# Kernel optimization log

Measured on AMD Instinct MI355X. Metric: run time of the kernel, lower is better.

Reference implementation:

```python
import jax, jax.numpy as jnp
import numpy as np

D_MODEL = 1024
N_HEADS = 32
HEAD_DIM = D_MODEL // N_HEADS
EPS = 1e-5


def setup_inputs() -> dict:
    key = jax.random.key(0)
    ks = jax.random.split(key, 6)
    B, S = 2, 2048
    scale = 1.0 / np.sqrt(D_MODEL)
    return {
        "x": jax.random.normal(ks[0], (B, S, D_MODEL), dtype=jnp.float32),
        "Wqkv_w": jax.random.normal(ks[1], (3 * D_MODEL, D_MODEL), dtype=jnp.float32) * scale,
        "Wqkv_b": jax.random.normal(ks[2], (3 * D_MODEL,), dtype=jnp.float32) * 0.01,
        "gn_w": jnp.ones((D_MODEL,), dtype=jnp.float32),
        "gn_b": jnp.zeros((D_MODEL,), dtype=jnp.float32),
        "out_w": jax.random.normal(ks[3], (D_MODEL, D_MODEL), dtype=jnp.float32) * scale,
        "out_b": jax.random.normal(ks[4], (D_MODEL,), dtype=jnp.float32) * 0.01,
    }


def reference(x, Wqkv_w, Wqkv_b, gn_w, gn_b, out_w, out_b):
    B, S, Dm = x.shape
    H, Dh = N_HEADS, HEAD_DIM
    # QKV projection
    qkv = x @ Wqkv_w.T + Wqkv_b                      # [B,S,3*Dm]
    qkv = qkv.reshape(B, S, 3, H, Dh)
    q, k, v = qkv[:, :, 0], qkv[:, :, 1], qkv[:, :, 2]  # each [B,S,H,Dh]
    # Linear (softmax-free) attention; dropout p=0 -> identity
    a = jnp.einsum('bthd,bshd->bhts', q, k)          # [B,H,S,S]
    ctx = jnp.einsum('bhts,bshd->bthd', a, v)        # [B,S,H,Dh]
    # GroupNorm(num_groups=H, num_channels=Dm) on transposed (B, Dm, S):
    # normalizes jointly over (Dh channels, S positions) per (batch, group)
    g = ctx.transpose(0, 2, 3, 1)                    # [B,H,Dh,S]
    mean = g.mean(axis=(2, 3), keepdims=True)
    var = ((g - mean) ** 2).mean(axis=(2, 3), keepdims=True)
    gh = (g - mean) * jax.lax.rsqrt(var + EPS)
    gh = gh * gn_w.reshape(H, Dh, 1) + gn_b.reshape(H, Dh, 1)
    ctx = gh.transpose(0, 3, 1, 2).reshape(B, S, Dm)  # back to [B,S,Dm]
    return ctx @ out_w.T + out_b
```

## Files before the change

### kernel.cpp

```cpp
#include <hip/hip_runtime.h>
#include <hip/hip_bf16.h>
#include <stdint.h>

typedef unsigned short ushort_t;
typedef __attribute__((ext_vector_type(4))) float f32x4;
typedef __attribute__((ext_vector_type(8))) short short8;

#define SS 2048
#define ROWS 4096
#define EPS 1e-5f

__device__ __forceinline__ unsigned short f2bf(float f) {
  unsigned int u = __float_as_uint(f);
  u += 0x7FFF + ((u >> 16) & 1);
  return (unsigned short)(u >> 16);
}
__device__ __forceinline__ float bf2f(short s) {
  return __uint_as_float(((unsigned int)(unsigned short)s) << 16);
}

#define GLDS16(g, l)                                                        \
  __builtin_amdgcn_global_load_lds((__attribute__((address_space(1))) void*)(g), \
                                   (__attribute__((address_space(3))) void*)(l), 16, 0, 0)

__global__ __launch_bounds__(256) void f2b3_kernel(const float* __restrict__ a,
                                                   ushort_t* __restrict__ oa, int n4a,
                                                   const float* __restrict__ b,
                                                   ushort_t* __restrict__ ob, int n4b,
                                                   const float* __restrict__ c,
                                                   ushort_t* __restrict__ oc, int n4c) {
  const int stride = gridDim.x * blockDim.x;
  const int total = n4a + n4b + n4c;
  for (int i = blockIdx.x * blockDim.x + threadIdx.x; i < total; i += stride) {
    const float* src; ushort_t* dst; int idx;
    if (i < n4a)            { src = a; dst = oa; idx = i; }
    else if (i < n4a + n4b) { src = b; dst = ob; idx = i - n4a; }
    else                    { src = c; dst = oc; idx = i - n4a - n4b; }
    const float4 v = reinterpret_cast<const float4*>(src)[idx];
    ushort4 o;
    o.x = f2bf(v.x); o.y = f2bf(v.y); o.z = f2bf(v.z); o.w = f2bf(v.w);
    reinterpret_cast<ushort4*>(dst)[idx] = o;
  }
}

#define MF(d, va, vb) d = __builtin_amdgcn_mfma_f32_16x16x32_bf16(va, vb, d, 0, 0, 0)
#define LD8(p) (*reinterpret_cast<const short8*>(p))

__global__ __launch_bounds__(512, 2) void gemm1_pipe(const ushort_t* __restrict__ A,
                                                     const ushort_t* __restrict__ B,
                                                     const float* __restrict__ bias,
                                                     ushort_t* __restrict__ C) {
  __shared__ __align__(16) ushort_t lds[4 * 14336];
  const int tid = threadIdx.x;
  const int wid = tid >> 6, lane = tid & 63;
  const int lin = blockIdx.x + (blockIdx.y << 4);
  const int xcd = lin & 7, idx = lin >> 3;
  const int bm = (((xcd & 3) << 2) + (idx & 3)) * 256;
  const int bn = (((xcd >> 2) << 3) + (idx >> 2)) * 192;
  const int wm = wid >> 2, wn = wid & 3;

  const int srow = lane >> 2;
  const int scol = ((lane & 3) ^ ((lane >> 3) & 3)) * 8;
  const int widb = (wid < 6) ? wid : 0;
  const ushort_t* gA0 = A + (size_t)(bm + wid * 16 + srow) * 1024 + scol;
  const ushort_t* gA1 = A + (size_t)(bm + (8 + wid) * 16 + srow) * 1024 + scol;
  const ushort_t* gB0 = B + (size_t)(bn + widb * 16 + srow) * 1024 + scol;
  const ushort_t* gB1 = B + (size_t)(bn + (6 + widb) * 16 + srow) * 1024 + scol;

  const int lf = lane & 15, kf = lane >> 4;
  const int flip = ((lane >> 1) & 3) << 4;
  const int aBase = (((wm * 128 + lf) * 64 + kf * 16) ^ flip) >> 1;
  const int bBase = ((((wn * 48 + lf) * 64 + kf * 16) ^ flip) >> 1) + 8192;

  f32x4 acc[8][3] = {};

#define STAGE_A(t)                                                           \
  { ushort_t* d = lds + (((t) & 3) * 14336);                                 \
    GLDS16(gA0 + (t) * 32, d + wid * 512);                                   \
    GLDS16(gA1 + (t) * 32, d + (8 + wid) * 512); }
#define STAGE_B(t)                                                           \
  if (wid < 6) { ushort_t* d = lds + (((t) & 3) * 14336) + 8192;             \
    GLDS16(gB0 + (t) * 32, d + wid * 512);                                   \
    GLDS16(gB1 + (t) * 32, d + (6 + wid) * 512); }

  STAGE_A(0) STAGE_B(0)
  STAGE_A(1) STAGE_B(1)
  STAGE_A(2) STAGE_B(2)
  if (wid < 6) { asm volatile("s_waitcnt vmcnt(8)" ::: "memory"); }
  else         { asm volatile("s_waitcnt vmcnt(4)" ::: "memory"); }
  __builtin_amdgcn_s_barrier();
  __builtin_amdgcn_sched_barrier(0);

#define K_TILE(t, DO_STAGE, VM6, VM2)                                        \
  { const ushort_t* Lb = lds + (((t) & 3) * 14336);                          \
    short8 bv0 = LD8(Lb + bBase);                                            \
    short8 bv1 = LD8(Lb + bBase + 512);                                      \
    short8 bv2 = LD8(Lb + bBase + 1024);                                     \
    short8 a0 = LD8(Lb + aBase);                                             \
    short8 a1 = LD8(Lb + aBase + 512);                                       \
    short8 a2 = LD8(Lb + aBase + 1024);                                      \
    short8 a3 = LD8(Lb + aBase + 1536);                                      \
    if (DO_STAGE) STAGE_A((t) + 3)                                           \
    __builtin_amdgcn_s_setprio(1);                                           \
    MF(acc[0][0], a0, bv0); MF(acc[1][0], a1, bv0);                          \
    MF(acc[0][1], a0, bv1); MF(acc[1][1], a1, bv1);                          \
    MF(acc[0][2], a0, bv2); MF(acc[1][2], a1, bv2);                          \
    MF(acc[2][0], a2, bv0); MF(acc[3][0], a3, bv0);                          \
    MF(acc[2][1], a2, bv1); MF(acc[3][1], a3, bv1);                          \
    MF(acc[2][2], a2, bv2); MF(acc[3][2], a3, bv2);                          \
    __builtin_amdgcn_s_setprio(0);                                           \
    a0 = LD8(Lb + aBase + 2048);                                             \
    a1 = LD8(Lb + aBase + 2560);                                             \
    a2 = LD8(Lb + aBase + 3072);                                             \
    a3 = LD8(Lb + aBase + 3584);                                             \
    if (DO_STAGE) STAGE_B((t) + 3)                                           \
    __builtin_amdgcn_s_setprio(1);                                           \
    MF(acc[4][0], a0, bv0); MF(acc[5][0], a1, bv0);                          \
    MF(acc[4][1], a0, bv1); MF(acc[5][1], a1, bv1);                          \
    MF(acc[4][2], a0, bv2); MF(acc[5][2], a1, bv2);                          \
    MF(acc[6][0], a2, bv0); MF(acc[7][0], a3, bv0);                          \
    MF(acc[6][1], a2, bv1); MF(acc[7][1], a3, bv1);                          \
    MF(acc[6][2], a2, bv2); MF(acc[7][2], a3, bv2);                          \
    __builtin_amdgcn_s_setprio(0);                                           \
    __builtin_amdgcn_sched_barrier(0);                                       \
    if (wid < 6) { asm volatile("s_waitcnt vmcnt(" #VM6 ")" ::: "memory"); } \
    else         { asm volatile("s_waitcnt vmcnt(" #VM2 ")" ::: "memory"); } \
    __builtin_amdgcn_s_barrier();                                            \
    __builtin_amdgcn_sched_barrier(0); }

#pragma unroll 1
  for (int t = 0; t < 29; ++t) K_TILE(t, 1, 8, 4)
  K_TILE(29, 0, 4, 2)
  K_TILE(30, 0, 0, 0)
  K_TILE(31, 0, 0, 0)

  const int crow = bm + wm * 128 + (lane >> 4) * 4;
  const int ccol = bn + wn * 48 + (lane & 15);
#pragma unroll
  for (int m = 0; m < 8; ++m)
#pragma unroll
    for (int n = 0; n < 3; ++n) {
      const int col = ccol + n * 16;
      const float bb = bias[col];
#pragma unroll
      for (int j = 0; j < 4; ++j)
        C[(size_t)(crow + m * 16 + j) * 3072 + col] = f2bf(acc[m][n][j] + bb);
    }
#undef K_TILE
#undef STAGE_A
#undef STAGE_B
}

__global__ __launch_bounds__(256, 2) void gemm2_pipe(const ushort_t* __restrict__ A,
                                                     const ushort_t* __restrict__ B,
                                                     const float* __restrict__ bias,
                                                     float* __restrict__ C) {
  __shared__ __align__(16) ushort_t lds[4 * 6144];
  const int tid = threadIdx.x;
  const int wid = tid >> 6, lane = tid & 63;
  const int bm = blockIdx.x * 64, bn = blockIdx.y * 128;
  const int wm = wid >> 1, wn = wid & 1;

  const int srow = lane >> 2;
  const int scol = ((lane & 3) ^ ((lane >> 3) & 3)) * 8;
  const ushort_t* gA  = A + (size_t)(bm + wid * 16 + srow) * 1024 + scol;
  const ushort_t* gB0 = B + (size_t)(bn + wid * 16 + srow) * 1024 + scol;
  const ushort_t* gB1 = B + (size_t)(bn + (4 + wid) * 16 + srow) * 1024 + scol;

  const int lf = lane & 15, kf = lane >> 4;
  const int flip = ((lane >> 1) & 3) << 4;
  const int aBase = (((wm * 32 + lf) * 64 + kf * 16) ^ flip) >> 1;
  const int bBase = ((((wn * 64 + lf) * 64 + kf * 16) ^ flip) >> 1) + 2048;

  f32x4 acc[2][4] = {};

#define STAGE2(t)                                                            \
  { ushort_t* d = lds + (((t) & 3) * 6144);                                  \
    GLDS16(gA + (t) * 32, d + wid * 512);                                    \
    GLDS16(gB0 + (t) * 32, d + 2048 + wid * 512);                            \
    GLDS16(gB1 + (t) * 32, d + 2048 + (4 + wid) * 512); }

  STAGE2(0) STAGE2(1) STAGE2(2)
  asm volatile("s_waitcnt vmcnt(6)" ::: "memory");
  __builtin_amdgcn_s_barrier();
  __builtin_amdgcn_sched_barrier(0);

#define K_TILE2(t, DO_STAGE, VM)                                             \
  { const ushort_t* Lb = lds + (((t) & 3) * 6144);                           \
    short8 bv0 = LD8(Lb + bBase);                                            \
    short8 bv1 = LD8(Lb + bBase + 512);                                      \
    short8 bv2 = LD8(Lb + bBase + 1024);                                     \
    short8 bv3 = LD8(Lb + bBase + 1536);                                     \
    short8 a0 = LD8(Lb + aBase);                                             \
    short8 a1 = LD8(Lb + aBase + 512);                                       \
    if (DO_STAGE) STAGE2((t) + 3)                                            \
    __builtin_amdgcn_s_setprio(1);                                           \
    MF(acc[0][0], a0, bv0); MF(acc[1][0], a1, bv0);                          \
    MF(acc[0][1], a0, bv1); MF(acc[1][1], a1, bv1);                          \
    MF(acc[0][2], a0, bv2); MF(acc[1][2], a1, bv2);                          \
    MF(acc[0][3], a0, bv3); MF(acc[1][3], a1, bv3);                          \
    __builtin_amdgcn_s_setprio(0);                                           \
    __builtin_amdgcn_sched_barrier(0);                                       \
    asm volatile("s_waitcnt vmcnt(" #VM ")" ::: "memory");                   \
    __builtin_amdgcn_s_barrier();                                            \
    __builtin_amdgcn_sched_barrier(0); }

#pragma unroll 1
  for (int t = 0; t < 29; ++t) K_TILE2(t, 1, 6)
  K_TILE2(29, 0, 3)
  K_TILE2(30, 0, 0)
  K_TILE2(31, 0, 0)

  const int crow = bm + wm * 32 + (lane >> 4) * 4;
  const int ccol = bn + wn * 64 + lf;
#pragma unroll
  for (int m = 0; m < 2; ++m)
#pragma unroll
    for (int n = 0; n < 4; ++n) {
      const int col = ccol + n * 16;
      const float bb = bias[col];
#pragma unroll
      for (int j = 0; j < 4; ++j)
        C[(size_t)(crow + m * 16 + j) * 1024 + col] = acc[m][n][j] + bb;
    }
#undef K_TILE2
#undef STAGE2
}

__global__ __launch_bounds__(256) void kvq_partial(const ushort_t* __restrict__ qkvb,
                                                   float* __restrict__ KVp,
                                                   float* __restrict__ Qcovp,
                                                   float* __restrict__ qsump) {
  __shared__ float qt[64 * 32];
  __shared__ float kt[64 * 32];
  __shared__ float vt[64 * 32];
  const int blk = blockIdx.x;
  const int bh = blk >> 5;
  const int ch = blk & 31;
  const int b = bh >> 5, h = bh & 31;
  const int tid = threadIdx.x;
  const int r = tid >> 2, cg = (tid & 3) * 8;
  const ushort_t* base = qkvb + (size_t)(b * SS + ch * 64 + r) * 3072 + h * 32 + cg;
  const short8 q8 = LD8(base);
  const short8 k8 = LD8(base + 1024);
  const short8 v8 = LD8(base + 2048);
#pragma unroll
  for (int i = 0; i < 8; ++i) {
    qt[r * 32 + cg + i] = bf2f(q8[i]);
    kt[r * 32 + cg + i] = bf2f(k8[i]);
    vt[r * 32 + cg + i] = bf2f(v8[i]);
  }
  __syncthreads();
  const int d = tid & 31, eg = tid >> 5;
  float kv[4] = {0.f, 0.f, 0.f, 0.f};
  float qc[4] = {0.f, 0.f, 0.f, 0.f};
#pragma unroll 4
  for (int ss = 0; ss < 64; ++ss) {
    const float vv = vt[ss * 32 + d];
    const float qd = qt[ss * 32 + d];
#pragma unroll
    for (int i = 0; i < 4; ++i) {
      kv[i] += kt[ss * 32 + eg * 4 + i] * vv;
      qc[i] += qt[ss * 32 + eg * 4 + i] * qd;
    }
  }
  float* okv = KVp + ((size_t)bh * 32 + ch) * 1024 + (eg * 4) * 32 + d;
  float* oqc = Qcovp + ((size_t)bh * 32 + ch) * 1024 + (eg * 4) * 32 + d;
#pragma unroll
  for (int i = 0; i < 4; ++i) { okv[i * 32] = kv[i]; oqc[i * 32] = qc[i]; }
  if (tid < 32) {
    float s = 0.f;
    for (int ss = 0; ss < 64; ++ss) s += qt[ss * 32 + tid];
    qsump[((size_t)bh * 32 + ch) * 32 + tid] = s;
  }
}

__global__ __launch_bounds__(256) void kvq_reduce_stats(const float* __restrict__ KVp,
                                                        const float* __restrict__ Qcovp,
                                                        const float* __restrict__ qsump,
                                                        float* __restrict__ KV,
                                                        float2* __restrict__ stats) {
  __shared__ float kvs[1024], qcov[1024], qsums[32], red[16];
  const int bh = blockIdx.x;
  const int tid = threadIdx.x;
  {
    const float* kbase = KVp + (size_t)bh * 32768 + tid * 4;
    const float* qbase = Qcovp + (size_t)bh * 32768 + tid * 4;
    float4 sk = make_float4(0.f, 0.f, 0.f, 0.f);
    float4 sq = make_float4(0.f, 0.f, 0.f, 0.f);
    for (int c = 0; c < 32; ++c) {
      const float4 k4 = *(const float4*)(kbase + c * 1024);
      const float4 q4 = *(const float4*)(qbase + c * 1024);
      sk.x += k4.x; sk.y += k4.y; sk.z += k4.z; sk.w += k4.w;
      sq.x += q4.x; sq.y += q4.y; sq.z += q4.z; sq.w += q4.w;
    }
    *(float4*)&kvs[tid * 4] = sk;
    *(float4*)&qcov[tid * 4] = sq;
    *(float4*)&KV[(size_t)bh * 1024 + tid * 4] = sk;
  }
  if (tid < 32) {
    float s = 0.f;
    for (int c = 0; c < 32; ++c) s += qsump[((size_t)bh * 32 + c) * 32 + tid];
    qsums[tid] = s;
  }
  __syncthreads();
  const int d = tid & 31, ig = tid >> 5;
  float e2p = 0.f;
#pragma unroll
  for (int ii = 0; ii < 4; ++ii) {
    const int i = ig * 4 + ii;
    float t = 0.f;
#pragma unroll
    for (int j = 0; j < 32; ++j) t += qcov[i * 32 + j] * kvs[j * 32 + d];
    e2p += kvs[i * 32 + d] * t;
  }
#pragma unroll
  for (int off = 32; off > 0; off >>= 1) e2p += __shfl_down(e2p, off);
  float mp = 0.f;
  if (tid < 32) {
    float rs = 0.f;
    for (int dd = 0; dd < 32; ++dd) rs += kvs[tid * 32 + ((dd + tid) & 31)];
    mp = rs * qsums[tid];
  }
#pragma unroll
  for (int off = 32; off > 0; off >>= 1) mp += __shfl_down(mp, off);
  const int wave = tid >> 6, lane = tid & 63;
  if (lane == 0) { red[wave] = e2p; red[8 + wave] = mp; }
  __syncthreads();
  if (tid == 0) {
    const float E2 = red[0] + red[1] + red[2] + red[3];
    const float MS = red[8] + red[9] + red[10] + red[11];
    const float mean = MS * (1.f / 65536.f);
    const float var = E2 * (1.f / 65536.f) - mean * mean;
    stats[bh] = make_float2(mean, rsqrtf(var + EPS));
  }
}

__global__ __launch_bounds__(256) void ctx_norm_kernel(const ushort_t* __restrict__ qkvb,
                                                       const float* __restrict__ KV,
                                                       const float2* __restrict__ stats,
                                                       const float* __restrict__ gw,
                                                       const float* __restrict__ gb,
                                                       ushort_t* __restrict__ ghb) {
  __shared__ float kvs[1024];
  __shared__ float gws[32], gbs[32];
  const int blk = blockIdx.x;
  const int bh = blk >> 3, tt = blk & 7;
  const int b = bh >> 5, h = bh & 31;
  const int tid = threadIdx.x;
  for (int i = tid; i < 1024; i += 256) kvs[i] = KV[(size_t)bh * 1024 + i];
  if (tid < 32) { gws[tid] = gw[h * 32 + tid]; gbs[tid] = gb[h * 32 + tid]; }
  const float2 st = stats[bh];
  __syncthreads();
  const float mean = st.x, rstd = st.y;
  const int t = tt * 256 + tid;
  const ushort_t* qrow = qkvb + ((size_t)(b * SS + t)) * 3072 + h * 32;
  float q[32];
#pragma unroll
  for (int g = 0; g < 4; ++g) {
    const short8 qv = LD8(qrow + g * 8);
#pragma unroll
    for (int i = 0; i < 8; ++i) q[g * 8 + i] = bf2f(qv[i]);
  }
  float o[32];
#pragma unroll
  for (int d = 0; d < 32; ++d) o[d] = 0.f;
#pragma unroll
  for (int e = 0; e < 32; ++e) {
    const float qe = q[e];
    const float* kr = &kvs[e * 32];
#pragma unroll
    for (int d = 0; d < 32; ++d) o[d] += qe * kr[d];
  }
  ushort_t* crow = ghb + ((size_t)(b * SS + t)) * 1024 + h * 32;
#pragma unroll
  for (int g = 0; g < 4; ++g) {
    short8 ov;
#pragma unroll
    for (int i = 0; i < 8; ++i) {
      const int d = g * 8 + i;
      ov[i] = (short)f2bf((o[d] - mean) * rstd * gws[d] + gbs[d]);
    }
    *(short8*)(crow + g * 8) = ov;
  }
}

extern "C" void kernel_launch(void* const* d_in, const int* in_sizes, int n_in,
                              void* d_out, int out_size, void* d_ws, size_t ws_size,
                              hipStream_t stream) {
  const float* x  = (const float*)d_in[0];
  const float* w1 = (const float*)d_in[1];
  const float* b1 = (const float*)d_in[2];
  const float* gw = (const float*)d_in[3];
  const float* gb = (const float*)d_in[4];
  const float* w2 = (const float*)d_in[5];
  const float* b2 = (const float*)d_in[6];
  float* out = (float*)d_out;

  char* ws = (char*)d_ws;
  ushort_t* Xb    = (ushort_t*)(ws);
  float*    KVp   = (float*)(ws);
  ushort_t* W1b   = (ushort_t*)(ws + 8388608);
  float*    Qcovp = (float*)(ws + 8388608);
  ushort_t* qkvb  = (ushort_t*)(ws + 16777216);
  ushort_t* ghb   = (ushort_t*)(ws + 41943040);
  ushort_t* W2b   = (ushort_t*)(ws + 50331648);
  float*    qsump = (float*)(ws + 52428800);
  float*    KV    = (float*)(ws + 52690944);
  float2*   stats = (float2*)(ws + 52953088);

  f2b3_kernel<<<2048, 256, 0, stream>>>(x, Xb, ROWS * 1024 / 4,
                                        w1, W1b, 3072 * 1024 / 4,
                                        w2, W2b, 1024 * 1024 / 4);
  gemm1_pipe<<<dim3(16, 16), 512, 0, stream>>>(Xb, W1b, b1, qkvb);
  kvq_partial<<<2048, 256, 0, stream>>>(qkvb, KVp, Qcovp, qsump);
  kvq_reduce_stats<<<64, 256, 0, stream>>>(KVp, Qcovp, qsump, KV, stats);
  ctx_norm_kernel<<<512, 256, 0, stream>>>(qkvb, KV, stats, gw, gb, ghb);
  gemm2_pipe<<<dim3(64, 8), 256, 0, stream>>>(ghb, W2b, b2, out);
}
```

Baseline: 93.45 us.

## Fuse KV/Qcov reduction into partial kernel via last-block atomic counter

Removes the separate kvq_reduce_stats launch: each partial block bumps a per-(batch,head) atomic counter after a threadfence, and the last of the 32 chunk blocks does the reduction and GroupNorm stats in place, reusing its shared memory. Counters are zeroed inside the conversion kernel. Separately, gemm1's XCD-aware block swizzle is replaced with plain blockIdx tiling. This saves one launch and its dependency gap, at the cost of a serialized tail in the last block per head and possibly worse cache locality in gemm1.

```diff
diff --git a/kernel.cpp b/kernel.cpp
--- a/kernel.cpp
+++ b/kernel.cpp
@@ -28,7 +28,9 @@
                                                    const float* __restrict__ b,
                                                    ushort_t* __restrict__ ob, int n4b,
                                                    const float* __restrict__ c,
-                                                   ushort_t* __restrict__ oc, int n4c) {
+                                                   ushort_t* __restrict__ oc, int n4c,
+                                                   unsigned int* __restrict__ cnt) {
+  if (blockIdx.x == 0 && threadIdx.x < 64) cnt[threadIdx.x] = 0;
   const int stride = gridDim.x * blockDim.x;
   const int total = n4a + n4b + n4c;
   for (int i = blockIdx.x * blockDim.x + threadIdx.x; i < total; i += stride) {
@@ -53,10 +55,7 @@
   __shared__ __align__(16) ushort_t lds[4 * 14336];
   const int tid = threadIdx.x;
   const int wid = tid >> 6, lane = tid & 63;
-  const int lin = blockIdx.x + (blockIdx.y << 4);
-  const int xcd = lin & 7, idx = lin >> 3;
-  const int bm = (((xcd & 3) << 2) + (idx & 3)) * 256;
-  const int bn = (((xcd >> 2) << 3) + (idx >> 2)) * 192;
+  const int bm = blockIdx.x * 256, bn = blockIdx.y * 192;
   const int wm = wid >> 2, wn = wid & 3;
 
   const int srow = lane >> 2;
@@ -230,10 +229,15 @@
 __global__ __launch_bounds__(256) void kvq_partial(const ushort_t* __restrict__ qkvb,
                                                    float* __restrict__ KVp,
                                                    float* __restrict__ Qcovp,
-                                                   float* __restrict__ qsump) {
-  __shared__ float qt[64 * 32];
-  __shared__ float kt[64 * 32];
-  __shared__ float vt[64 * 32];
+                                                   float* __restrict__ qsump,
+                                                   float* __restrict__ KV,
+                                                   float2* __restrict__ stats,
+                                                   unsigned int* __restrict__ cnt) {
+  __shared__ float smem[3 * 2048];
+  float* qt = smem;
+  float* kt = smem + 2048;
+  float* vt = smem + 4096;
+  __shared__ unsigned int sdone;
   const int blk = blockIdx.x;
   const int bh = blk >> 5;
   const int ch = blk & 31;
@@ -273,16 +277,14 @@
     for (int ss = 0; ss < 64; ++ss) s += qt[ss * 32 + tid];
     qsump[((size_t)bh * 32 + ch) * 32 + tid] = s;
   }
-}
-
-__global__ __launch_bounds__(256) void kvq_reduce_stats(const float* __restrict__ KVp,
-                                                        const float* __restrict__ Qcovp,
-                                                        const float* __restrict__ qsump,
-                                                        float* __restrict__ KV,
-                                                        float2* __restrict__ stats) {
-  __shared__ float kvs[1024], qcov[1024], qsums[32], red[16];
-  const int bh = blockIdx.x;
-  const int tid = threadIdx.x;
+  __threadfence();
+  __syncthreads();
+  if (tid == 0) sdone = atomicAdd(&cnt[bh], 1u);
+  __syncthreads();
+  if (sdone != 31u) return;
+  __threadfence();
+  float* kvs = qt;
+  float* qcov = kt;
   {
     const float* kbase = KVp + (size_t)bh * 32768 + tid * 4;
     const float* qbase = Qcovp + (size_t)bh * 32768 + tid * 4;
@@ -294,6 +296,7 @@
       sk.x += k4.x; sk.y += k4.y; sk.z += k4.z; sk.w += k4.w;
       sq.x += q4.x; sq.y += q4.y; sq.z += q4.z; sq.w += q4.w;
     }
+    __syncthreads();
     *(float4*)&kvs[tid * 4] = sk;
     *(float4*)&qcov[tid * 4] = sq;
     *(float4*)&KV[(size_t)bh * 1024 + tid * 4] = sk;
@@ -301,10 +304,10 @@
   if (tid < 32) {
     float s = 0.f;
     for (int c = 0; c < 32; ++c) s += qsump[((size_t)bh * 32 + c) * 32 + tid];
-    qsums[tid] = s;
-  }
-  __syncthreads();
-  const int d = tid & 31, ig = tid >> 5;
+    vt[tid] = s;
+  }
+  __syncthreads();
+  const int ig = tid >> 5;
   float e2p = 0.f;
 #pragma unroll
   for (int ii = 0; ii < 4; ++ii) {
@@ -320,16 +323,16 @@
   if (tid < 32) {
     float rs = 0.f;
     for (int dd = 0; dd < 32; ++dd) rs += kvs[tid * 32 + ((dd + tid) & 31)];
-    mp = rs * qsums[tid];
+    mp = rs * vt[tid];
   }
 #pragma unroll
   for (int off = 32; off > 0; off >>= 1) mp += __shfl_down(mp, off);
   const int wave = tid >> 6, lane = tid & 63;
-  if (lane == 0) { red[wave] = e2p; red[8 + wave] = mp; }
+  if (lane == 0) { vt[32 + wave] = e2p; vt[40 + wave] = mp; }
   __syncthreads();
   if (tid == 0) {
-    const float E2 = red[0] + red[1] + red[2] + red[3];
-    const float MS = red[8] + red[9] + red[10] + red[11];
+    const float E2 = vt[32] + vt[33] + vt[34] + vt[35];
+    const float MS = vt[40] + vt[41] + vt[42] + vt[43];
     const float mean = MS * (1.f / 65536.f);
     const float var = E2 * (1.f / 65536.f) - mean * mean;
     stats[bh] = make_float2(mean, rsqrtf(var + EPS));
@@ -408,13 +411,13 @@
   float*    qsump = (float*)(ws + 52428800);
   float*    KV    = (float*)(ws + 52690944);
   float2*   stats = (float2*)(ws + 52953088);
+  unsigned int* cnt = (unsigned int*)(ws + 52954112);
 
   f2b3_kernel<<<2048, 256, 0, stream>>>(x, Xb, ROWS * 1024 / 4,
                                         w1, W1b, 3072 * 1024 / 4,
-                                        w2, W2b, 1024 * 1024 / 4);
+                                        w2, W2b, 1024 * 1024 / 4, cnt);
   gemm1_pipe<<<dim3(16, 16), 512, 0, stream>>>(Xb, W1b, b1, qkvb);
-  kvq_partial<<<2048, 256, 0, stream>>>(qkvb, KVp, Qcovp, qsump);
-  kvq_reduce_stats<<<64, 256, 0, stream>>>(KVp, Qcovp, qsump, KV, stats);
+  kvq_partial<<<2048, 256, 0, stream>>>(qkvb, KVp, Qcovp, qsump, KV, stats, cnt);
   ctx_norm_kernel<<<512, 256, 0, stream>>>(qkvb, KV, stats, gw, gb, ghb);
   gemm2_pipe<<<dim3(64, 8), 256, 0, stream>>>(ghb, W2b, b2, out);
 }
```

After: 348.3 us. 3.73x slower.
